# Kernel optimization log

Measured on AMD Instinct MI355X. Metric: run time of the kernel, lower is better.

Reference implementation:

```python
import jax, jax.numpy as jnp
import numpy as np

NX, NY = 8192, 8192
C1, C2, D = 2048, 2048, 512

def setup_inputs() -> dict:
    key = jax.random.key(0)
    k1, k2, k3, k4, k5 = jax.random.split(key, 5)
    scale1 = 1.0 / np.sqrt(C1)
    scale2 = 1.0 / np.sqrt(C2)
    return {
        "x": jax.random.normal(k1, (NX, C1), dtype=jnp.float32),
        "y": jax.random.normal(k2, (NY, C2), dtype=jnp.float32),
        "Wq": jax.random.uniform(k3, (D, C1), dtype=jnp.float32, minval=-scale1, maxval=scale1),
        "Wk": jax.random.uniform(k4, (D, C2), dtype=jnp.float32, minval=-scale2, maxval=scale2),
        "Wv": jax.random.uniform(k5, (D, C2), dtype=jnp.float32, minval=-scale2, maxval=scale2),
    }

def reference(x, y, Wq, Wk, Wv):
    d = Wq.shape[0]
    q = x @ Wq.T                      # [nx, d]
    k = y @ Wk.T                      # [ny, d]
    v = y @ Wv.T                      # [ny, d]
    a = (q @ k.T) * (d ** -0.5)       # [nx, ny]
    # torch.triu(ones) masks upper triangle INCLUDING diagonal -> zero where j >= i
    nx, ny = a.shape
    i = jnp.arange(nx)[:, None]
    j = jnp.arange(ny)[None, :]
    a = jnp.where(j >= i, 0.0, a)
    return a @ v                      # [nx, d]
```

## Files before the change

kernel.cpp:

```cpp
#include <hip/hip_runtime.h>
#include <hip/hip_bf16.h>


typedef __bf16 bf16x8 __attribute__((ext_vector_type(8)));
typedef __bf16 bf16x4 __attribute__((ext_vector_type(4)));
typedef float f32x4 __attribute__((ext_vector_type(4)));

#define MFMA16(a, b, c) __builtin_amdgcn_mfma_f32_16x16x32_bf16(a, b, c, 0, 0, 0)

constexpr float SCALE = 0.04419417382415922f;

__device__ __forceinline__ void ld16(const void* g, void* l) {
    __builtin_amdgcn_global_load_lds(
        (__attribute__((address_space(1))) void*)g,
        (__attribute__((address_space(3))) void*)l, 16, 0, 0);
}

__device__ __forceinline__ bf16x8 frag(const __bf16* base, int r, int c) {
    return *(const bf16x8*)((const char*)base + r * 128 + ((c ^ (r & 7)) * 16));
}

__device__ __forceinline__ bf16x8 fragA32(const float* base, int r, int c0) {
    const char* rowp = (const char*)base + r * 256;
    f32x4 a = *(const f32x4*)(rowp + ((c0 ^ (r & 15)) * 16));
    f32x4 b = *(const f32x4*)(rowp + (((c0 + 1) ^ (r & 15)) * 16));
    bf16x8 o;
    o[0] = (__bf16)a[0]; o[1] = (__bf16)a[1];
    o[2] = (__bf16)a[2]; o[3] = (__bf16)a[3];
    o[4] = (__bf16)b[0]; o[5] = (__bf16)b[1];
    o[6] = (__bf16)b[2]; o[7] = (__bf16)b[3];
    return o;
}

__device__ inline bf16x4 pack4(float4 a) {
    bf16x4 r;
    r[0] = (__bf16)a.x; r[1] = (__bf16)a.y;
    r[2] = (__bf16)a.z; r[3] = (__bf16)a.w;
    return r;
}

__global__ __launch_bounds__(256) void convert_w(
    const float* __restrict__ wqf, const float* __restrict__ wkf,
    const float* __restrict__ wvf, __bf16* __restrict__ wqb,
    __bf16* __restrict__ wkb, __bf16* __restrict__ wvb)
{
    const size_t tid = (size_t)blockIdx.x * 256 + threadIdx.x;
    const size_t w = tid >> 6;
    const int lane = (int)(tid & 63);
    size_t f = w * 512;
    const float* src; __bf16* dst;
    if (f < 1048576)      { src = wqf; dst = wqb; }
    else if (f < 2097152) { src = wkf; dst = wkb; f -= 1048576; }
    else                  { src = wvf; dst = wvb; f -= 2097152; }
    const float4* s4 = (const float4*)(src + f);
    float4 a = s4[lane];
    float4 b = s4[64 + lane];
    __bf16* d = dst + f;
    *(bf16x4*)(d + lane * 4)       = pack4(a);
    *(bf16x4*)(d + 256 + lane * 4) = pack4(b);
}

__global__ __launch_bounds__(256, 3) void gemm_qkv_fused(
    const float* __restrict__ x, const float* __restrict__ y,
    const __bf16* __restrict__ wq, const __bf16* __restrict__ wk,
    const __bf16* __restrict__ wv, __bf16* __restrict__ qo,
    __bf16* __restrict__ ko, __bf16* __restrict__ vo)
{
    constexpr int K = 2048, N = 512;
    __shared__ __align__(16) float  Asf[128][64];
    __shared__ __align__(16) __bf16 Bs[128][64];

    const int z = blockIdx.z;
    const float* A = (z == 0) ? x : y;
    const __bf16* B = (z == 0) ? wq : (z == 1) ? wk : wv;
    __bf16* C = (z == 0) ? qo : (z == 1) ? ko : vo;
    const float mul = (z == 0) ? SCALE : 1.0f;

    const int tid  = threadIdx.x;
    const int wave = tid >> 6, lane = tid & 63;
    const int fr = lane & 15, fq = lane >> 4;
    const int m0 = blockIdx.x * 128, n0 = blockIdx.y * 128;
    const int wr = (wave >> 1) * 64, wc = (wave & 1) * 64;
    const int lr = lane >> 3;
    const int cd = (lane & 7) ^ lr;
    const int lr4 = lane >> 4;
    const int cl  = lane & 15;

    f32x4 acc[4][4];
#pragma unroll
    for (int a = 0; a < 4; ++a)
#pragma unroll
        for (int b = 0; b < 4; ++b) acc[a][b] = f32x4{0.f, 0.f, 0.f, 0.f};

    const __bf16* bg = B + (size_t)(n0 + wave * 32 + lr) * K + cd * 8;
    float*  alf = &Asf[wave * 32][0];
    __bf16* bl  = &Bs[wave * 32][0];
    const float* ag0 = A + (size_t)(m0 + wave * 32 + lr4) * K;

    for (int kk = 0; kk < K; kk += 64) {
        __syncthreads();
#pragma unroll
        for (int u = 0; u < 4; ++u)
            ld16(bg + (size_t)(u * 8) * K + kk, bl + u * 512);
#pragma unroll
        for (int u = 0; u < 8; ++u) {
            const int rw = u * 4 + lr4;
            const int c  = cl ^ (rw & 15);
            ld16(ag0 + (size_t)(u * 4) * K + kk + c * 4, alf + u * 256);
        }
        __syncthreads();
#pragma unroll
        for (int ks = 0; ks < 2; ++ks) {
            bf16x8 af[4], bf[4];
#pragma unroll
            for (int rt = 0; rt < 4; ++rt)
                af[rt] = fragA32(&Asf[0][0], wr + rt * 16 + fr, ks * 8 + fq * 2);
#pragma unroll
            for (int nt = 0; nt < 4; ++nt)
                bf[nt] = frag(&Bs[0][0], wc + nt * 16 + fr, ks * 4 + fq);
#pragma unroll
            for (int rt = 0; rt < 4; ++rt)
#pragma unroll
                for (int nt = 0; nt < 4; ++nt)
                    acc[rt][nt] = MFMA16(af[rt], bf[nt], acc[rt][nt]);
        }
    }

#pragma unroll
    for (int rt = 0; rt < 4; ++rt)
#pragma unroll
        for (int nt = 0; nt < 4; ++nt) {
            const int col = n0 + wc + nt * 16 + fr;
#pragma unroll
            for (int r = 0; r < 4; ++r) {
                const int row = m0 + wr + rt * 16 + fq * 4 + r;
                C[(size_t)row * N + col] = (__bf16)(acc[rt][nt][r] * mul);
            }
        }
}

__global__ __launch_bounds__(256) void transpose_v(
    const ushort* __restrict__ v, ushort* __restrict__ vT)
{
    __shared__ ushort tile[64][72];
    const int t = threadIdx.x;
    const int r0 = blockIdx.x * 64;
    const int c0 = blockIdx.y * 64;
    const int lr = t >> 2;
    const int lc = (t & 3) * 16;

    union { float4 f[2]; ushort s[16]; } u;
    const float4* vp = (const float4*)(v + (size_t)(r0 + lr) * 512 + c0 + lc);
    u.f[0] = vp[0];
    u.f[1] = vp[1];
#pragma unroll
    for (int e = 0; e < 16; ++e) tile[lc + e][lr] = u.s[e];
    __syncthreads();
    float4* op = (float4*)(vT + (size_t)(c0 + lr) * 8192 + r0 + lc);
    op[0] = *(const float4*)&tile[lr][lc];
    op[1] = *(const float4*)&tile[lr][lc + 8];
}

__global__ __launch_bounds__(256, 3) void h_gemm(
    const __bf16* __restrict__ vT, const __bf16* __restrict__ kT,
    __bf16* __restrict__ Ht)
{
    __shared__ __align__(16) __bf16 As[128][64];
    __shared__ __align__(16) __bf16 Bs[128][64];

    const int c  = blockIdx.y;
    const int m0 = (blockIdx.x & 3) * 128;
    const int n0 = (blockIdx.x >> 2) * 128;

    const int tid  = threadIdx.x;
    const int wave = tid >> 6, lane = tid & 63;
    const int fr = lane & 15, fq = lane >> 4;
    const int wr = (wave >> 1) * 64, wc = (wave & 1) * 64;
    const int lr = lane >> 3;
    const int cd = (lane & 7) ^ lr;

    f32x4 acc[4][4];
#pragma unroll
    for (int a = 0; a < 4; ++a)
#pragma unroll
        for (int b = 0; b < 4; ++b) acc[a][b] = f32x4{0.f, 0.f, 0.f, 0.f};

    const __bf16* ag = vT + (size_t)(m0 + wave * 32 + lr) * 8192 + c * 128 + cd * 8;
    const __bf16* bg = kT + (size_t)(n0 + wave * 32 + lr) * 8192 + c * 128 + cd * 8;
    __bf16* al = &As[wave * 32][0];
    __bf16* bl = &Bs[wave * 32][0];

    for (int kk = 0; kk < 128; kk += 64) {
        __syncthreads();
#pragma unroll
        for (int u = 0; u < 4; ++u) {
            ld16(ag + (size_t)(u * 8) * 8192 + kk, al + u * 512);
            ld16(bg + (size_t)(u * 8) * 8192 + kk, bl + u * 512);
        }
        __syncthreads();
#pragma unroll
        for (int ks = 0; ks < 2; ++ks) {
            bf16x8 af[4], bf[4];
#pragma unroll
            for (int rt = 0; rt < 4; ++rt)
                af[rt] = frag(&As[0][0], wr + rt * 16 + fr, ks * 4 + fq);
#pragma unroll
            for (int nt = 0; nt < 4; ++nt)
                bf[nt] = frag(&Bs[0][0], wc + nt * 16 + fr, ks * 4 + fq);
#pragma unroll
            for (int rt = 0; rt < 4; ++rt)
#pragma unroll
                for (int nt = 0; nt < 4; ++nt)
                    acc[rt][nt] = MFMA16(af[rt], bf[nt], acc[rt][nt]);
        }
    }

    __bf16* tp = Ht + (size_t)c * 262144;
#pragma unroll
    for (int rt = 0; rt < 4; ++rt)
#pragma unroll
        for (int nt = 0; nt < 4; ++nt) {
            const int col = n0 + wc + nt * 16 + fr;
#pragma unroll
            for (int r = 0; r < 4; ++r) {
                const int row = m0 + wr + rt * 16 + fq * 4 + r;
                tp[(size_t)row * 512 + col] = (__bf16)acc[rt][nt][r];
            }
        }
}

__global__ __launch_bounds__(256) void prefix_scan(
    const __bf16* __restrict__ Ht, __bf16* __restrict__ Pt)
{
    const size_t e = ((size_t)blockIdx.x * 256 + threadIdx.x) * 4;
    float a0 = 0.f, a1 = 0.f, a2 = 0.f, a3 = 0.f;
#pragma unroll 7
    for (int c = 0; c < 63; ++c) {
        bf16x4 h = *(const bf16x4*)(Ht + (size_t)c * 262144 + e);
        a0 += (float)h[0]; a1 += (float)h[1];
        a2 += (float)h[2]; a3 += (float)h[3];
        bf16x4 p;
        p[0] = (__bf16)a0; p[1] = (__bf16)a1;
        p[2] = (__bf16)a2; p[3] = (__bf16)a3;
        *(bf16x4*)(Pt + (size_t)(c + 1) * 262144 + e) = p;
    }
}

__global__ __launch_bounds__(256, 3) void s_diag(
    const __bf16* __restrict__ q, const __bf16* __restrict__ k,
    __bf16* __restrict__ Sd)
{
    constexpr int K = 512;
    __shared__ __align__(16) __bf16 As[128][64];
    __shared__ __align__(16) __bf16 Bs[128][64];

    const int t = blockIdx.x;

    const int tid  = threadIdx.x;
    const int wave = tid >> 6, lane = tid & 63;
    const int fr = lane & 15, fq = lane >> 4;
    const int wr = (wave >> 1) * 64, wc = (wave & 1) * 64;
    const int lr = lane >> 3;
    const int cd = (lane & 7) ^ lr;

    f32x4 acc[4][4];
#pragma unroll
    for (int a = 0; a < 4; ++a)
#pragma unroll
        for (int b = 0; b < 4; ++b) acc[a][b] = f32x4{0.f, 0.f, 0.f, 0.f};

    const __bf16* ag = q + (size_t)(t * 128 + wave * 32 + lr) * K + cd * 8;
    const __bf16* bg = k + (size_t)(t * 128 + wave * 32 + lr) * K + cd * 8;
    __bf16* al = &As[wave * 32][0];
    __bf16* bl = &Bs[wave * 32][0];

    for (int kk = 0; kk < K; kk += 64) {
        __syncthreads();
#pragma unroll
        for (int u = 0; u < 4; ++u) {
            ld16(ag + (size_t)(u * 8) * K + kk, al + u * 512);
            ld16(bg + (size_t)(u * 8) * K + kk, bl + u * 512);
        }
        __syncthreads();
#pragma unroll
        for (int ks = 0; ks < 2; ++ks) {
            bf16x8 af[4], bf[4];
#pragma unroll
            for (int rt = 0; rt < 4; ++rt)
                af[rt] = frag(&As[0][0], wr + rt * 16 + fr, ks * 4 + fq);
#pragma unroll
            for (int nt = 0; nt < 4; ++nt)
                bf[nt] = frag(&Bs[0][0], wc + nt * 16 + fr, ks * 4 + fq);
#pragma unroll
            for (int rt = 0; rt < 4; ++rt)
#pragma unroll
                for (int nt = 0; nt < 4; ++nt)
                    acc[rt][nt] = MFMA16(af[rt], bf[nt], acc[rt][nt]);
        }
    }

    __bf16* tp = Sd + (size_t)t * 16384;
#pragma unroll
    for (int rt = 0; rt < 4; ++rt)
#pragma unroll
        for (int nt = 0; nt < 4; ++nt) {
            const int col = wc + nt * 16 + fr;
#pragma unroll
            for (int r = 0; r < 4; ++r) {
                const int row = wr + rt * 16 + fq * 4 + r;
                float vv = (col < row) ? acc[rt][nt][r] : 0.f;
                tp[row * 128 + col] = (__bf16)vv;
            }
        }
}

__global__ __launch_bounds__(256, 3) void out_gemm(
    const __bf16* __restrict__ q, const __bf16* __restrict__ Sd,
    const __bf16* __restrict__ vT, const __bf16* __restrict__ Pt,
    float* __restrict__ out)
{
    __shared__ __align__(16) __bf16 As[128][64];
    __shared__ __align__(16) __bf16 Bs[128][64];

    const int t  = blockIdx.x;
    const int n0 = blockIdx.y * 128;

    const int tid  = threadIdx.x;
    const int wave = tid >> 6, lane = tid & 63;
    const int fr = lane & 15, fq = lane >> 4;
    const int wr = (wave >> 1) * 64, wc = (wave & 1) * 64;
    const int lr = lane >> 3;
    const int cd = (lane & 7) ^ lr;
    const int srow = wave * 32 + lr;

    f32x4 acc[4][4];
#pragma unroll
    for (int a = 0; a < 4; ++a)
#pragma unroll
        for (int b = 0; b < 4; ++b) acc[a][b] = f32x4{0.f, 0.f, 0.f, 0.f};

    __bf16* al = &As[wave * 32][0];
    __bf16* bl = &Bs[wave * 32][0];

    if (t > 0) {
        const __bf16* ag = q + (size_t)(t * 128 + srow) * 512 + cd * 8;
        const __bf16* bg2 = Pt + (size_t)t * 262144
                          + (size_t)(n0 + srow) * 512 + cd * 8;
        for (int kk = 0; kk < 512; kk += 64) {
            __syncthreads();
#pragma unroll
            for (int u = 0; u < 4; ++u) {
                ld16(ag + (size_t)(u * 8) * 512 + kk, al + u * 512);
                ld16(bg2 + (size_t)(u * 8) * 512 + kk, bl + u * 512);
            }
            __syncthreads();
#pragma unroll
            for (int ks = 0; ks < 2; ++ks) {
                bf16x8 af[4], bf[4];
#pragma unroll
                for (int rt = 0; rt < 4; ++rt)
                    af[rt] = frag(&As[0][0], wr + rt * 16 + fr, ks * 4 + fq);
#pragma unroll
                for (int nt = 0; nt < 4; ++nt)
                    bf[nt] = frag(&Bs[0][0], wc + nt * 16 + fr, ks * 4 + fq);
#pragma unroll
                for (int rt = 0; rt < 4; ++rt)
#pragma unroll
                    for (int nt = 0; nt < 4; ++nt)
                        acc[rt][nt] = MFMA16(af[rt], bf[nt], acc[rt][nt]);
            }
        }
    }

    const __bf16* at3 = Sd + (size_t)t * 16384 + (size_t)srow * 128 + cd * 8;
    const __bf16* bg3 = vT + (size_t)(n0 + srow) * 8192 + t * 128 + cd * 8;
    for (int kk = 0; kk < 128; kk += 64) {
        __syncthreads();
#pragma unroll
        for (int u = 0; u < 4; ++u) {
            ld16(at3 + (size_t)(u * 8) * 128 + kk, al + u * 512);
            ld16(bg3 + (size_t)(u * 8) * 8192 + kk, bl + u * 512);
        }
        __syncthreads();
#pragma unroll
        for (int ks = 0; ks < 2; ++ks) {
            bf16x8 af[4], bf[4];
#pragma unroll
            for (int rt = 0; rt < 4; ++rt)
                af[rt] = frag(&As[0][0], wr + rt * 16 + fr, ks * 4 + fq);
#pragma unroll
            for (int nt = 0; nt < 4; ++nt)
                bf[nt] = frag(&Bs[0][0], wc + nt * 16 + fr, ks * 4 + fq);
#pragma unroll
            for (int rt = 0; rt < 4; ++rt)
#pragma unroll
                for (int nt = 0; nt < 4; ++nt)
                    acc[rt][nt] = MFMA16(af[rt], bf[nt], acc[rt][nt]);
        }
    }

#pragma unroll
    for (int rt = 0; rt < 4; ++rt)
#pragma unroll
        for (int nt = 0; nt < 4; ++nt) {
            const int col = n0 + wc + nt * 16 + fr;
#pragma unroll
            for (int r = 0; r < 4; ++r) {
                const int row = t * 128 + wr + rt * 16 + fq * 4 + r;
                out[(size_t)row * 512 + col] = acc[rt][nt][r];
            }
        }
}

extern "C" void kernel_launch(void* const* d_in, const int* in_sizes, int n_in,
                              void* d_out, int out_size, void* d_ws, size_t ws_size,
                              hipStream_t stream) {
    const float* x  = (const float*)d_in[0];
    const float* y  = (const float*)d_in[1];
    const float* Wq = (const float*)d_in[2];
    const float* Wk = (const float*)d_in[3];
    const float* Wv = (const float*)d_in[4];
    float* out = (float*)d_out;

    const size_t QK = (size_t)8192 * 512;
    __bf16* q  = (__bf16*)d_ws;
    __bf16* k  = q + QK;
    __bf16* v  = k + QK;
    __bf16* vT = v + QK;
    __bf16* Ht  = vT + QK;
    __bf16* Pt  = Ht + 16777216;
    __bf16* wqb = Pt + 16777216;
    __bf16* wkb = wqb + 1048576;
    __bf16* wvb = wkb + 1048576;
    __bf16* kT = v;
    __bf16* Sd = wqb;

    convert_w<<<1536, 256, 0, stream>>>(Wq, Wk, Wv, wqb, wkb, wvb);
    gemm_qkv_fused<<<dim3(64, 4, 3), 256, 0, stream>>>(x, y, wqb, wkb, wvb, q, k, v);
    transpose_v<<<dim3(128, 8), 256, 0, stream>>>((const ushort*)v, (ushort*)vT);
    transpose_v<<<dim3(128, 8), 256, 0, stream>>>((const ushort*)k, (ushort*)kT);
    h_gemm<<<dim3(16, 63), 256, 0, stream>>>(vT, kT, Ht);
    s_diag<<<64, 256, 0, stream>>>(q, k, Sd);
    prefix_scan<<<256, 256, 0, stream>>>(Ht, Pt);
    out_gemm<<<dim3(64, 4), 256, 0, stream>>>(q, Sd, vT, Pt, out);
}
```

Before: 283.0 us.

## Fuse K/V projections sharing y tiles, write transposes in epilogue, merge h_gemm with s_diag

The QKV projection kernel now has blocks for y compute K and V together from one shared y tile, using two accumulator sets and loading y once for both. K and V are also written transposed straight from the epilogue, which removes the two separate transpose kernels. The diagonal score computation is folded into the chunked H GEMM as extra grid rows, cutting launches and filling the machine better. In exchange, register pressure rises (launch bounds drop to 2 waves), Q blocks sit idle during the V half, the transposed stores are 8-byte scattered writes, and the grid becomes imbalanced between Q and KV blocks.

```diff
diff --git a/kernel.cpp b/kernel.cpp
--- a/kernel.cpp
+++ b/kernel.cpp
@@ -60,48 +60,57 @@
     *(bf16x4*)(d + 256 + lane * 4) = pack4(b);
 }
 
-__global__ __launch_bounds__(256, 3) void gemm_qkv_fused(
+__global__ __launch_bounds__(256, 2) void gemm_qkv2(
     const float* __restrict__ x, const float* __restrict__ y,
     const __bf16* __restrict__ wq, const __bf16* __restrict__ wk,
     const __bf16* __restrict__ wv, __bf16* __restrict__ qo,
-    __bf16* __restrict__ ko, __bf16* __restrict__ vo)
+    __bf16* __restrict__ ko, __bf16* __restrict__ kT,
+    __bf16* __restrict__ vT)
 {
     constexpr int K = 2048, N = 512;
     __shared__ __align__(16) float  Asf[128][64];
-    __shared__ __align__(16) __bf16 Bs[128][64];
-
-    const int z = blockIdx.z;
-    const float* A = (z == 0) ? x : y;
-    const __bf16* B = (z == 0) ? wq : (z == 1) ? wk : wv;
-    __bf16* C = (z == 0) ? qo : (z == 1) ? ko : vo;
-    const float mul = (z == 0) ? SCALE : 1.0f;
+    __shared__ __align__(16) __bf16 Bs[2][128][64];
+
+    const bool iskv = (blockIdx.y & 1) != 0;
+    const float* A = iskv ? y : x;
+    const __bf16* B0 = iskv ? wk : wq;
 
     const int tid  = threadIdx.x;
     const int wave = tid >> 6, lane = tid & 63;
     const int fr = lane & 15, fq = lane >> 4;
-    const int m0 = blockIdx.x * 128, n0 = blockIdx.y * 128;
+    const int m0 = blockIdx.x * 128, n0 = (blockIdx.y >> 1) * 128;
     const int wr = (wave >> 1) * 64, wc = (wave & 1) * 64;
     const int lr = lane >> 3;
     const int cd = (lane & 7) ^ lr;
     const int lr4 = lane >> 4;
     const int cl  = lane & 15;
 
-    f32x4 acc[4][4];
+    f32x4 acc0[4][4], acc1[4][4];
 #pragma unroll
     for (int a = 0; a < 4; ++a)
 #pragma unroll
-        for (int b = 0; b < 4; ++b) acc[a][b] = f32x4{0.f, 0.f, 0.f, 0.f};
-
-    const __bf16* bg = B + (size_t)(n0 + wave * 32 + lr) * K + cd * 8;
+        for (int b = 0; b < 4; ++b) {
+            acc0[a][b] = f32x4{0.f, 0.f, 0.f, 0.f};
+            acc1[a][b] = f32x4{0.f, 0.f, 0.f, 0.f};
+        }
+
+    const __bf16* bg0 = B0 + (size_t)(n0 + wave * 32 + lr) * K + cd * 8;
+    const __bf16* bg1 = wv + (size_t)(n0 + wave * 32 + lr) * K + cd * 8;
     float*  alf = &Asf[wave * 32][0];
-    __bf16* bl  = &Bs[wave * 32][0];
+    __bf16* bl0 = &Bs[0][wave * 32][0];
+    __bf16* bl1 = &Bs[1][wave * 32][0];
     const float* ag0 = A + (size_t)(m0 + wave * 32 + lr4) * K;
 
     for (int kk = 0; kk < K; kk += 64) {
         __syncthreads();
 #pragma unroll
         for (int u = 0; u < 4; ++u)
-            ld16(bg + (size_t)(u * 8) * K + kk, bl + u * 512);
+            ld16(bg0 + (size_t)(u * 8) * K + kk, bl0 + u * 512);
+        if (iskv) {
+#pragma unroll
+            for (int u = 0; u < 4; ++u)
+                ld16(bg1 + (size_t)(u * 8) * K + kk, bl1 + u * 512);
+        }
 #pragma unroll
         for (int u = 0; u < 8; ++u) {
             const int rw = u * 4 + lr4;
@@ -117,60 +126,65 @@
                 af[rt] = fragA32(&Asf[0][0], wr + rt * 16 + fr, ks * 8 + fq * 2);
 #pragma unroll
             for (int nt = 0; nt < 4; ++nt)
-                bf[nt] = frag(&Bs[0][0], wc + nt * 16 + fr, ks * 4 + fq);
+                bf[nt] = frag(&Bs[0][0][0], wc + nt * 16 + fr, ks * 4 + fq);
 #pragma unroll
             for (int rt = 0; rt < 4; ++rt)
 #pragma unroll
                 for (int nt = 0; nt < 4; ++nt)
-                    acc[rt][nt] = MFMA16(af[rt], bf[nt], acc[rt][nt]);
-        }
-    }
-
-#pragma unroll
-    for (int rt = 0; rt < 4; ++rt)
-#pragma unroll
-        for (int nt = 0; nt < 4; ++nt) {
-            const int col = n0 + wc + nt * 16 + fr;
-#pragma unroll
-            for (int r = 0; r < 4; ++r) {
-                const int row = m0 + wr + rt * 16 + fq * 4 + r;
-                C[(size_t)row * N + col] = (__bf16)(acc[rt][nt][r] * mul);
-            }
-        }
-}
-
-__global__ __launch_bounds__(256) void transpose_v(
-    const ushort* __restrict__ v, ushort* __restrict__ vT)
-{
-    __shared__ ushort tile[64][72];
-    const int t = threadIdx.x;
-    const int r0 = blockIdx.x * 64;
-    const int c0 = blockIdx.y * 64;
-    const int lr = t >> 2;
-    const int lc = (t & 3) * 16;
-
-    union { float4 f[2]; ushort s[16]; } u;
-    const float4* vp = (const float4*)(v + (size_t)(r0 + lr) * 512 + c0 + lc);
-    u.f[0] = vp[0];
-    u.f[1] = vp[1];
-#pragma unroll
-    for (int e = 0; e < 16; ++e) tile[lc + e][lr] = u.s[e];
-    __syncthreads();
-    float4* op = (float4*)(vT + (size_t)(c0 + lr) * 8192 + r0 + lc);
-    op[0] = *(const float4*)&tile[lr][lc];
-    op[1] = *(const float4*)&tile[lr][lc + 8];
-}
-
-__global__ __launch_bounds__(256, 3) void h_gemm(
+                    acc0[rt][nt] = MFMA16(af[rt], bf[nt], acc0[rt][nt]);
+            if (iskv) {
+                bf16x8 bg[4];
+#pragma unroll
+                for (int nt = 0; nt < 4; ++nt)
+                    bg[nt] = frag(&Bs[1][0][0], wc + nt * 16 + fr, ks * 4 + fq);
+#pragma unroll
+                for (int rt = 0; rt < 4; ++rt)
+#pragma unroll
+                    for (int nt = 0; nt < 4; ++nt)
+                        acc1[rt][nt] = MFMA16(af[rt], bg[nt], acc1[rt][nt]);
+            }
+        }
+    }
+
+    if (!iskv) {
+#pragma unroll
+        for (int rt = 0; rt < 4; ++rt)
+#pragma unroll
+            for (int nt = 0; nt < 4; ++nt) {
+                const int col = n0 + wc + nt * 16 + fr;
+#pragma unroll
+                for (int r = 0; r < 4; ++r) {
+                    const int row = m0 + wr + rt * 16 + fq * 4 + r;
+                    qo[(size_t)row * N + col] = (__bf16)(acc0[rt][nt][r] * SCALE);
+                }
+            }
+    } else {
+#pragma unroll
+        for (int rt = 0; rt < 4; ++rt)
+#pragma unroll
+            for (int nt = 0; nt < 4; ++nt) {
+                const int col  = n0 + wc + nt * 16 + fr;
+                const int row0 = m0 + wr + rt * 16 + fq * 4;
+                bf16x4 k4, v4;
+#pragma unroll
+                for (int r = 0; r < 4; ++r) {
+                    k4[r] = (__bf16)acc0[rt][nt][r];
+                    v4[r] = (__bf16)acc1[rt][nt][r];
+                    ko[(size_t)(row0 + r) * N + col] = k4[r];
+                }
+                *(bf16x4*)(kT + (size_t)col * 8192 + row0) = k4;
+                *(bf16x4*)(vT + (size_t)col * 8192 + row0) = v4;
+            }
+    }
+}
+
+__global__ __launch_bounds__(256, 3) void hs_gemm(
     const __bf16* __restrict__ vT, const __bf16* __restrict__ kT,
-    __bf16* __restrict__ Ht)
+    const __bf16* __restrict__ q, const __bf16* __restrict__ k,
+    __bf16* __restrict__ Ht, __bf16* __restrict__ Sd)
 {
     __shared__ __align__(16) __bf16 As[128][64];
     __shared__ __align__(16) __bf16 Bs[128][64];
-
-    const int c  = blockIdx.y;
-    const int m0 = (blockIdx.x & 3) * 128;
-    const int n0 = (blockIdx.x >> 2) * 128;
 
     const int tid  = threadIdx.x;
     const int wave = tid >> 6, lane = tid & 63;
@@ -185,48 +199,99 @@
 #pragma unroll
         for (int b = 0; b < 4; ++b) acc[a][b] = f32x4{0.f, 0.f, 0.f, 0.f};
 
-    const __bf16* ag = vT + (size_t)(m0 + wave * 32 + lr) * 8192 + c * 128 + cd * 8;
-    const __bf16* bg = kT + (size_t)(n0 + wave * 32 + lr) * 8192 + c * 128 + cd * 8;
     __bf16* al = &As[wave * 32][0];
     __bf16* bl = &Bs[wave * 32][0];
 
-    for (int kk = 0; kk < 128; kk += 64) {
-        __syncthreads();
-#pragma unroll
-        for (int u = 0; u < 4; ++u) {
-            ld16(ag + (size_t)(u * 8) * 8192 + kk, al + u * 512);
-            ld16(bg + (size_t)(u * 8) * 8192 + kk, bl + u * 512);
-        }
-        __syncthreads();
-#pragma unroll
-        for (int ks = 0; ks < 2; ++ks) {
-            bf16x8 af[4], bf[4];
-#pragma unroll
-            for (int rt = 0; rt < 4; ++rt)
-                af[rt] = frag(&As[0][0], wr + rt * 16 + fr, ks * 4 + fq);
-#pragma unroll
-            for (int nt = 0; nt < 4; ++nt)
-                bf[nt] = frag(&Bs[0][0], wc + nt * 16 + fr, ks * 4 + fq);
-#pragma unroll
-            for (int rt = 0; rt < 4; ++rt)
-#pragma unroll
-                for (int nt = 0; nt < 4; ++nt)
-                    acc[rt][nt] = MFMA16(af[rt], bf[nt], acc[rt][nt]);
-        }
-    }
-
-    __bf16* tp = Ht + (size_t)c * 262144;
-#pragma unroll
-    for (int rt = 0; rt < 4; ++rt)
-#pragma unroll
-        for (int nt = 0; nt < 4; ++nt) {
-            const int col = n0 + wc + nt * 16 + fr;
-#pragma unroll
-            for (int r = 0; r < 4; ++r) {
-                const int row = m0 + wr + rt * 16 + fq * 4 + r;
-                tp[(size_t)row * 512 + col] = (__bf16)acc[rt][nt][r];
-            }
-        }
+    if (blockIdx.y < 63) {
+        const int c  = blockIdx.y;
+        const int m0 = (blockIdx.x & 3) * 128;
+        const int n0 = (blockIdx.x >> 2) * 128;
+
+        const __bf16* ag = vT + (size_t)(m0 + wave * 32 + lr) * 8192 + c * 128 + cd * 8;
+        const __bf16* bg = kT + (size_t)(n0 + wave * 32 + lr) * 8192 + c * 128 + cd * 8;
+
+        for (int kk = 0; kk < 128; kk += 64) {
+            __syncthreads();
+#pragma unroll
+            for (int u = 0; u < 4; ++u) {
+                ld16(ag + (size_t)(u * 8) * 8192 + kk, al + u * 512);
+                ld16(bg + (size_t)(u * 8) * 8192 + kk, bl + u * 512);
+            }
+            __syncthreads();
+#pragma unroll
+            for (int ks = 0; ks < 2; ++ks) {
+                bf16x8 af[4], bf[4];
+#pragma unroll
+                for (int rt = 0; rt < 4; ++rt)
+                    af[rt] = frag(&As[0][0], wr + rt * 16 + fr, ks * 4 + fq);
+#pragma unroll
+                for (int nt = 0; nt < 4; ++nt)
+                    bf[nt] = frag(&Bs[0][0], wc + nt * 16 + fr, ks * 4 + fq);
+#pragma unroll
+                for (int rt = 0; rt < 4; ++rt)
+#pragma unroll
+                    for (int nt = 0; nt < 4; ++nt)
+                        acc[rt][nt] = MFMA16(af[rt], bf[nt], acc[rt][nt]);
+            }
+        }
+
+        __bf16* tp = Ht + (size_t)c * 262144;
+#pragma unroll
+        for (int rt = 0; rt < 4; ++rt)
+#pragma unroll
+            for (int nt = 0; nt < 4; ++nt) {
+                const int col = n0 + wc + nt * 16 + fr;
+#pragma unroll
+                for (int r = 0; r < 4; ++r) {
+                    const int row = m0 + wr + rt * 16 + fq * 4 + r;
+                    tp[(size_t)row * 512 + col] = (__bf16)acc[rt][nt][r];
+                }
+            }
+    } else {
+        const int t = (blockIdx.y - 63) * 16 + blockIdx.x;
+
+        const __bf16* ag = q + (size_t)(t * 128 + wave * 32 + lr) * 512 + cd * 8;
+        const __bf16* bg = k + (size_t)(t * 128 + wave * 32 + lr) * 512 + cd * 8;
+
+        for (int kk = 0; kk < 512; kk += 64) {
+            __syncthreads();
+#pragma unroll
+            for (int u = 0; u < 4; ++u) {
+                ld16(ag + (size_t)(u * 8) * 512 + kk, al + u * 512);
+                ld16(bg + (size_t)(u * 8) * 512 + kk, bl + u * 512);
+            }
+            __syncthreads();
+#pragma unroll
+            for (int ks = 0; ks < 2; ++ks) {
+                bf16x8 af[4], bf[4];
+#pragma unroll
+                for (int rt = 0; rt < 4; ++rt)
+                    af[rt] = frag(&As[0][0], wr + rt * 16 + fr, ks * 4 + fq);
+#pragma unroll
+                for (int nt = 0; nt < 4; ++nt)
+                    bf[nt] = frag(&Bs[0][0], wc + nt * 16 + fr, ks * 4 + fq);
+#pragma unroll
+                for (int rt = 0; rt < 4; ++rt)
+#pragma unroll
+                    for (int nt = 0; nt < 4; ++nt)
+                        acc[rt][nt] = MFMA16(af[rt], bf[nt], acc[rt][nt]);
+            }
+        }
+
+        __bf16* tp = Sd + (size_t)t * 16384;
+#pragma unroll
+        for (int rt = 0; rt < 4; ++rt)
+#pragma unroll
+            for (int nt = 0; nt < 4; ++nt) {
+                const int col = wc + nt * 16 + fr;
+#pragma unroll
+                for (int r = 0; r < 4; ++r) {
+                    const int row = wr + rt * 16 + fq * 4 + r;
+                    float vv = (col < row) ? acc[rt][nt][r] : 0.f;
+                    tp[row * 128 + col] = (__bf16)vv;
+                }
+            }
+    }
 }
 
 __global__ __launch_bounds__(256) void prefix_scan(
@@ -246,74 +311,6 @@
     }
 }
 
-__global__ __launch_bounds__(256, 3) void s_diag(
-    const __bf16* __restrict__ q, const __bf16* __restrict__ k,
-    __bf16* __restrict__ Sd)
-{
-    constexpr int K = 512;
-    __shared__ __align__(16) __bf16 As[128][64];
-    __shared__ __align__(16) __bf16 Bs[128][64];
-
-    const int t = blockIdx.x;
-
-    const int tid  = threadIdx.x;
-    const int wave = tid >> 6, lane = tid & 63;
-    const int fr = lane & 15, fq = lane >> 4;
-    const int wr = (wave >> 1) * 64, wc = (wave & 1) * 64;
-    const int lr = lane >> 3;
-    const int cd = (lane & 7) ^ lr;
-
-    f32x4 acc[4][4];
-#pragma unroll
-    for (int a = 0; a < 4; ++a)
-#pragma unroll
-        for (int b = 0; b < 4; ++b) acc[a][b] = f32x4{0.f, 0.f, 0.f, 0.f};
-
-    const __bf16* ag = q + (size_t)(t * 128 + wave * 32 + lr) * K + cd * 8;
-    const __bf16* bg = k + (size_t)(t * 128 + wave * 32 + lr) * K + cd * 8;
-    __bf16* al = &As[wave * 32][0];
-    __bf16* bl = &Bs[wave * 32][0];
-
-    for (int kk = 0; kk < K; kk += 64) {
-        __syncthreads();
-#pragma unroll
-        for (int u = 0; u < 4; ++u) {
-            ld16(ag + (size_t)(u * 8) * K + kk, al + u * 512);
-            ld16(bg + (size_t)(u * 8) * K + kk, bl + u * 512);
-        }
-        __syncthreads();
-#pragma unroll
-        for (int ks = 0; ks < 2; ++ks) {
-            bf16x8 af[4], bf[4];
-#pragma unroll
-            for (int rt = 0; rt < 4; ++rt)
-                af[rt] = frag(&As[0][0], wr + rt * 16 + fr, ks * 4 + fq);
-#pragma unroll
-            for (int nt = 0; nt < 4; ++nt)
-                bf[nt] = frag(&Bs[0][0], wc + nt * 16 + fr, ks * 4 + fq);
-#pragma unroll
-            for (int rt = 0; rt < 4; ++rt)
-#pragma unroll
-                for (int nt = 0; nt < 4; ++nt)
-                    acc[rt][nt] = MFMA16(af[rt], bf[nt], acc[rt][nt]);
-        }
-    }
-
-    __bf16* tp = Sd + (size_t)t * 16384;
-#pragma unroll
-    for (int rt = 0; rt < 4; ++rt)
-#pragma unroll
-        for (int nt = 0; nt < 4; ++nt) {
-            const int col = wc + nt * 16 + fr;
-#pragma unroll
-            for (int r = 0; r < 4; ++r) {
-                const int row = wr + rt * 16 + fq * 4 + r;
-                float vv = (col < row) ? acc[rt][nt][r] : 0.f;
-                tp[row * 128 + col] = (__bf16)vv;
-            }
-        }
-}
-
 __global__ __launch_bounds__(256, 3) void out_gemm(
     const __bf16* __restrict__ q, const __bf16* __restrict__ Sd,
     const __bf16* __restrict__ vT, const __bf16* __restrict__ Pt,
@@ -425,22 +422,18 @@
     const size_t QK = (size_t)8192 * 512;
     __bf16* q  = (__bf16*)d_ws;
     __bf16* k  = q + QK;
-    __bf16* v  = k + QK;
-    __bf16* vT = v + QK;
+    __bf16* kT = k + QK;
+    __bf16* vT = kT + QK;
     __bf16* Ht  = vT + QK;
     __bf16* Pt  = Ht + 16777216;
     __bf16* wqb = Pt + 16777216;
     __bf16* wkb = wqb + 1048576;
     __bf16* wvb = wkb + 1048576;
-    __bf16* kT = v;
     __bf16* Sd = wqb;
 
     convert_w<<<1536, 256, 0, stream>>>(Wq, Wk, Wv, wqb, wkb, wvb);
-    gemm_qkv_fused<<<dim3(64, 4, 3), 256, 0, stream>>>(x, y, wqb, wkb, wvb, q, k, v);
-    transpose_v<<<dim3(128, 8), 256, 0, stream>>>((const ushort*)v, (ushort*)vT);
-    transpose_v<<<dim3(128, 8), 256, 0, stream>>>((const ushort*)k, (ushort*)kT);
-    h_gemm<<<dim3(16, 63), 256, 0, stream>>>(vT, kT, Ht);
-    s_diag<<<64, 256, 0, stream>>>(q, k, Sd);
+    gemm_qkv2<<<dim3(64, 8), 256, 0, stream>>>(x, y, wqb, wkb, wvb, q, k, kT, vT);
+    hs_gemm<<<dim3(16, 67), 256, 0, stream>>>(vT, kT, q, k, Ht, Sd);
     prefix_scan<<<256, 256, 0, stream>>>(Ht, Pt);
     out_gemm<<<dim3(64, 4), 256, 0, stream>>>(q, Sd, vT, Pt, out);
 }
```

After: 254.7 us. -10.0%, faster.
